# Kernel optimization log

Hardware: AMD Instinct MI355X
Metric: run time of the kernel (lower is better)

## Reference

```python
import jax, jax.numpy as jnp
import numpy as np

EPS = 1e-3  # tfa GroupNormalization default epsilon
H = 8       # num heads


def group_norm(x, gamma, beta):
    # x: [..., E]; per-sample group norm over each group of head_dim channels
    lead, E = x.shape[:-1], x.shape[-1]
    D = E // H
    xg = x.reshape(lead + (H, D))
    mu = xg.mean(-1, keepdims=True)
    var = xg.var(-1, keepdims=True)
    xg = (xg - mu) * jax.lax.rsqrt(var + EPS)
    xg = xg * gamma.reshape(H, D) + beta.reshape(H, D)
    return xg.reshape(lead + (E,))


def in_proj(x, W, b, gamma, beta):
    # Dense -> CELU(alpha=1) == ELU -> GroupNorm(groups=H)
    return group_norm(jax.nn.elu(x @ W + b), gamma, beta)


def setup_inputs() -> dict:
    B, M, E, MID = 16, 2048, 1024, 64
    D = E // H
    ks = jax.random.split(jax.random.key(0), 16)
    w = lambda k, shape: jax.random.normal(k, shape, jnp.float32) * 0.02
    inp = {
        "query": jax.random.normal(ks[0], (B, E), jnp.float32),
        "key": jax.random.normal(ks[1], (B * M, E), jnp.float32),
        "mask": jnp.ones((B, M), jnp.float32),
        "value1": jax.random.normal(ks[2], (B, E), jnp.float32),
        "value2": jax.random.normal(ks[3], (B * M, E), jnp.float32),
        # four in-projection layers: Dense(E,E) + GroupNorm gamma/beta
        "Wq": w(ks[4], (E, E)), "bq": jnp.zeros((E,), jnp.float32), "gq": jnp.ones((E,), jnp.float32), "Bq": jnp.zeros((E,), jnp.float32),
        "Wk": w(ks[5], (E, E)), "bk": jnp.zeros((E,), jnp.float32), "gk": jnp.ones((E,), jnp.float32), "Bk": jnp.zeros((E,), jnp.float32),
        "Wv1": w(ks[6], (E, E)), "bv1": jnp.zeros((E,), jnp.float32), "gv1": jnp.ones((E,), jnp.float32), "Bv1": jnp.zeros((E,), jnp.float32),
        "Wv2": w(ks[7], (E, E)), "bv2": jnp.zeros((E,), jnp.float32), "gv2": jnp.ones((E,), jnp.float32), "Bv2": jnp.zeros((E,), jnp.float32),
        # XLASCAtt: basic Dense(head_dim->64)+ReLU; last Dense(64->1); last2 Dense(64->head_dim)
        "Wb": w(ks[8], (D, MID)), "bb": jnp.zeros((MID,), jnp.float32),
        "Wl1": w(ks[9], (MID, 1)), "bl1": jnp.zeros((1,), jnp.float32),
        "Wl2": w(ks[10], (MID, D)), "bl2": jnp.zeros((D,), jnp.float32),
    }
    return inp


def reference(query, key, mask, value1, value2,
              Wq, bq, gq, Bq, Wk, bk, gk, Bk,
              Wv1, bv1, gv1, Bv1, Wv2, bv2, gv2, Bv2,
              Wb, bb, Wl1, bl1, Wl2, bl2):
    B, E = query.shape
    D = E // H
    # in-projections
    q = in_proj(query, Wq, bq, gq, Bq).reshape(B, H, D)            # [B,H,D]
    v1 = in_proj(value1, Wv1, bv1, gv1, Bv1).reshape(B, H, D)      # [B,H,D]
    k = in_proj(key, Wk, bk, gk, Bk).reshape(B, -1, H, D).transpose(0, 2, 1, 3)       # [B,H,M,D]
    v2 = in_proj(value2, Wv2, bv2, gv2, Bv2).reshape(B, -1, H, D).transpose(0, 2, 1, 3)  # [B,H,M,D]

    # low-rank bilinear attention map: elementwise q*k per head
    att_map = q[:, :, None, :] * k                                 # [B,H,M,D]
    basic = jax.nn.relu(att_map @ Wb + bb)                         # [B,H,M,MID]

    # masked mean-pool over memory positions
    m_ext = mask[:, None, :, None]                                 # [B,1,M,1]
    pool = (basic * m_ext).sum(-2) / m_ext.sum(-2)                 # [B,H,MID]

    # spatial attention (softmax over M) and channel gate (sigmoid)
    alpha_sp = (basic @ Wl1 + bl1)[..., 0]                         # [B,H,M]
    alpha_sp = jnp.where(mask[:, None, :] == 0, -1e9, alpha_sp)
    alpha_sp = jax.nn.softmax(alpha_sp, axis=-1)
    alpha_ch = jax.nn.sigmoid(pool @ Wl2 + bl2)                    # [B,H,D]

    v2_agg = jnp.einsum('bhm,bhmd->bhd', alpha_sp, v2)             # [B,H,D]
    attn = v1 * v2_agg * alpha_ch                                  # [B,H,D]
    return attn.reshape(B, H * D)
```

## Files before the change

### kernel.cpp

```cpp
#include <hip/hip_runtime.h>
#include <hip/hip_bf16.h>
#include <math.h>

typedef __attribute__((ext_vector_type(8))) short bf16x8;
typedef __attribute__((ext_vector_type(4))) float f32x4;
typedef __attribute__((ext_vector_type(8))) unsigned short u16x8;

typedef const float* fptr;
typedef const unsigned short* bfp;

__device__ inline float b2f(unsigned short u) {
    union { unsigned int i; float f; } v; v.i = ((unsigned int)u) << 16; return v.f;
}
__device__ inline unsigned short f2b(float x) {
    __hip_bfloat16 h = __float2bfloat16(x);
    return *(unsigned short*)&h;
}
__device__ inline float elu_f(float x) { return x > 0.f ? x : __expf(x) - 1.f; }

__device__ inline void load_lds16(const void* g, void* l) {
    __builtin_amdgcn_global_load_lds(
        (const __attribute__((address_space(1))) unsigned int*)g,
        (__attribute__((address_space(3))) unsigned int*)l, 16, 0, 0);
}

__global__ __launch_bounds__(256) void prep(
    fptr Wk, fptr Wv2, unsigned short* WtK, unsigned short* WtV2,
    fptr Wb, unsigned short* Wbt,
    fptr query, fptr Wq, fptr bq, fptr gq, fptr Bq,
    fptr value1, fptr Wv1, fptr bv1, fptr gv1, fptr Bv1,
    float* qws, float* v1ws)
{
    __shared__ __align__(16) char smem[16640];
    int blk = blockIdx.x, t = threadIdx.x;

    if (blk == 0) {
        unsigned short* tb = (unsigned short*)smem;
        for (int i = 0; i < 32; i++) {
            int idx = i * 256 + t;
            tb[(idx & 63) * 128 + (idx >> 6)] = f2b(Wb[idx]);
        }
        __syncthreads();
        for (int i = 0; i < 4; i++) {
            int o = (i * 256 + t) * 8;
            *(u16x8*)&Wbt[o] = *(const u16x8*)&tb[o];
        }
        return;
    }
    if (blk < 257) {
        float* xs = (float*)smem;
        float (*part)[128] = (float (*)[128])(smem + 4096);
        float (*r4)[2] = (float (*)[2])(smem + 4096 + 1024);
        int idx = blk - 1;
        int hgrp = idx & 7;
        int row  = (idx >> 3) & 15;
        int which = idx >> 7;
        fptr x  = which ? value1 : query;
        fptr W  = which ? Wv1 : Wq;
        fptr bi = which ? bv1 : bq;
        fptr g  = which ? gv1 : gq;
        fptr be = which ? Bv1 : Bq;
        float* outp = which ? v1ws : qws;
        int lane = t & 63, wv = t >> 6;
        for (int i = t; i < 1024; i += 256) xs[i] = x[row * 1024 + i];
        __syncthreads();
        int cl = t & 127, kh = t >> 7;
        int col = hgrp * 128 + cl;
        float acc = 0.f;
        const float* wp = W + (size_t)(kh * 512) * 1024 + col;
        for (int k = 0; k < 512; k++) acc += xs[kh * 512 + k] * wp[(size_t)k * 1024];
        part[kh][cl] = acc;
        __syncthreads();
        float e = 0.f;
        if (t < 128) e = elu_f(part[0][t] + part[1][t] + bi[col]);
        float s = e, ss = e * e;
        for (int m = 32; m > 0; m >>= 1) { s += __shfl_xor(s, m); ss += __shfl_xor(ss, m); }
        if (lane == 0) { r4[wv][0] = s; r4[wv][1] = ss; }
        __syncthreads();
        float S  = r4[0][0] + r4[1][0] + r4[2][0] + r4[3][0];
        float SS = r4[0][1] + r4[1][1] + r4[2][1] + r4[3][1];
        float mean = S * (1.f / 128.f);
        float var  = SS * (1.f / 128.f) - mean * mean;
        float inv  = rsqrtf(var + 1e-3f);
        if (t < 128) outp[row * 1024 + col] = (e - mean) * inv * g[col] + be[col];
        return;
    }
    {
        float (*tl)[65] = (float (*)[65])smem;
        int idx = blk - 257;
        fptr W = (idx >> 8) ? Wv2 : Wk;
        unsigned short* Wt = (idx >> 8) ? WtV2 : WtK;
        int k0 = ((idx >> 4) & 15) * 64, n0 = (idx & 15) * 64;
        #pragma unroll
        for (int i = 0; i < 16; i++) {
            int kl = i * 4 + (t >> 6), nl = t & 63;
            tl[kl][nl] = W[(size_t)(k0 + kl) * 1024 + n0 + nl];
        }
        __syncthreads();
        #pragma unroll
        for (int i = 0; i < 2; i++) {
            int nl = i * 32 + (t >> 3), kl8 = (t & 7) * 8;
            u16x8 o;
            #pragma unroll
            for (int e = 0; e < 8; e++) o[e] = f2b(tl[kl8 + e][nl]);
            *(u16x8*)&Wt[(size_t)(n0 + nl) * 1024 + k0 + kl8] = o;
        }
    }
}

__global__ __launch_bounds__(256, 4) void gemm_fused(
    fptr AKf, bfp WtK, fptr bkp, fptr gkp, fptr Bkp,
    fptr AVf, bfp WtV, fptr bvp, fptr gvp, fptr Bvp,
    bfp Wbt, const float* qws, fptr maskp, fptr bbp, fptr Wl1, fptr bl1,
    float* logits, float* poolpart, __hip_bfloat16* Z)
{
    __shared__ __align__(16) unsigned short pool[17408];
    unsigned short (*As)[128][32] = (unsigned short (*)[128][32])pool;
    unsigned short (*Bs)[128][32] = (unsigned short (*)[128][32])(pool + 8192);
    unsigned short (*Tt)[136]     = (unsigned short (*)[136])pool;
    __shared__ float sstat[128][2][2];
    __shared__ float masksh[128];
    __shared__ float poolred[4][64];

    int bid = blockIdx.x;
    int xcd = bid & 7;
    int seq = bid >> 3;
    int grp = seq >> 3;
    int h   = seq & 7;
    int which = grp >> 5;
    int rowtile = xcd * 32 + (grp & 31);

    int r0 = rowtile * 128;
    int n0 = h * 128;
    int b  = r0 >> 11;
    int mloc = r0 & 2047;
    int mt = rowtile & 15;
    int t = threadIdx.x, lane = t & 63, w = t >> 6;
    int c = lane & 15, q = lane >> 4;
    int rowbase = (w & 1) * 64, colbase = (w >> 1) * 64;

    fptr Af   = which ? AVf : AKf;
    bfp Wt    = which ? WtV : WtK;
    fptr bias = which ? bvp : bkp;
    fptr g    = which ? gvp : gkp;
    fptr be   = which ? Bvp : Bkp;

    if (which == 0 && t < 128) masksh[t] = maskp[r0 + t];

    f32x4 acc[4][4];
    const f32x4 fzero = {0.f, 0.f, 0.f, 0.f};
    #pragma unroll
    for (int i = 0; i < 4; i++)
        #pragma unroll
        for (int j = 0; j < 4; j++) acc[i][j] = fzero;

    int srow = lane >> 2;
    int sseg = (lane & 3) * 8;
    const float* agf = Af + (size_t)(r0 + w * 32 + srow) * 1024 + sseg;
    const unsigned short* bg = Wt + (size_t)(n0 + w * 32 + srow) * 1024 + sseg;

    for (int k0 = 0; k0 < 1024; k0 += 64) {
        load_lds16(bg + k0,                  &Bs[0][w * 32][0]);
        load_lds16(bg + k0 + 16 * 1024,      &Bs[0][w * 32 + 16][0]);
        load_lds16(bg + k0 + 32,             &Bs[1][w * 32][0]);
        load_lds16(bg + k0 + 32 + 16 * 1024, &Bs[1][w * 32 + 16][0]);
        #pragma unroll
        for (int ch = 0; ch < 4; ch++) {
            const float* src = agf + k0 + (ch & 1) * 16 * 1024 + (ch >> 1) * 32;
            float4 f0 = *(const float4*)src;
            float4 f1 = *(const float4*)(src + 4);
            u16x8 hv = { f2b(f0.x), f2b(f0.y), f2b(f0.z), f2b(f0.w),
                         f2b(f1.x), f2b(f1.y), f2b(f1.z), f2b(f1.w) };
            *(u16x8*)&As[ch >> 1][w * 32 + (ch & 1) * 16 + srow][sseg] = hv;
        }
        __syncthreads();
        #pragma unroll
        for (int p = 0; p < 2; p++) {
            bf16x8 af[4], bfv[4];
            #pragma unroll
            for (int i = 0; i < 4; i++) af[i]  = *(const bf16x8*)&As[p][rowbase + i * 16 + c][q * 8];
            #pragma unroll
            for (int j = 0; j < 4; j++) bfv[j] = *(const bf16x8*)&Bs[p][colbase + j * 16 + c][q * 8];
            #pragma unroll
            for (int i = 0; i < 4; i++)
                #pragma unroll
                for (int j = 0; j < 4; j++)
                    acc[i][j] = __builtin_amdgcn_mfma_f32_16x16x32_bf16(af[i], bfv[j], acc[i][j], 0, 0, 0);
        }
        __syncthreads();
    }

    float bcol[4], gcol[4], Bcol[4];
    #pragma unroll
    for (int j = 0; j < 4; j++) {
        int cg = n0 + colbase + j * 16 + c;
        bcol[j] = bias[cg]; gcol[j] = g[cg]; Bcol[j] = be[cg];
    }
    #pragma unroll
    for (int i = 0; i < 4; i++)
        #pragma unroll
        for (int j = 0; j < 4; j++)
            #pragma unroll
            for (int r = 0; r < 4; r++)
                acc[i][j][r] = elu_f(acc[i][j][r] + bcol[j]);
    #pragma unroll
    for (int i = 0; i < 4; i++) {
        #pragma unroll
        for (int r = 0; r < 4; r++) {
            float s  = acc[i][0][r] + acc[i][1][r] + acc[i][2][r] + acc[i][3][r];
            float ss = acc[i][0][r] * acc[i][0][r] + acc[i][1][r] * acc[i][1][r]
                     + acc[i][2][r] * acc[i][2][r] + acc[i][3][r] * acc[i][3][r];
            for (int m = 1; m < 16; m <<= 1) { s += __shfl_xor(s, m); ss += __shfl_xor(ss, m); }
            if (c == 0) {
                int rl = rowbase + i * 16 + q * 4 + r;
                sstat[rl][w >> 1][0] = s;
                sstat[rl][w >> 1][1] = ss;
            }
        }
    }
    __syncthreads();
    #pragma unroll
    for (int i = 0; i < 4; i++) {
        #pragma unroll
        for (int r = 0; r < 4; r++) {
            int rl = rowbase + i * 16 + q * 4 + r;
            float S  = sstat[rl][0][0] + sstat[rl][1][0];
            float SS = sstat[rl][0][1] + sstat[rl][1][1];
            float mean = S * (1.f / 128.f);
            float var  = SS * (1.f / 128.f) - mean * mean;
            float inv  = rsqrtf(var + 1e-3f);
            #pragma unroll
            for (int j = 0; j < 4; j++) {
                int cl = colbase + j * 16 + c;
                float v = (acc[i][j][r] - mean) * inv * gcol[j] + Bcol[j];
                Tt[rl][cl] = f2b(v);
            }
        }
    }
    __syncthreads();
    if (which != 0) {
        unsigned short* Zu = (unsigned short*)Z;
        #pragma unroll
        for (int i = 0; i < 8; i++) {
            int idx2 = i * 256 + t;
            int row = idx2 >> 4, ch = (idx2 & 15) * 8;
            *(u16x8*)&Zu[(size_t)(r0 + row) * 1024 + n0 + ch] = *(const u16x8*)&Tt[row][ch];
        }
        return;
    }

    const float* qrow = qws + b * 1024 + h * 128;
    f32x4 acc2[2][4];
    #pragma unroll
    for (int i = 0; i < 2; i++)
        #pragma unroll
        for (int j = 0; j < 4; j++) acc2[i][j] = fzero;
    #pragma unroll
    for (int s = 0; s < 4; s++) {
        bf16x8 af2[2], bfv[4];
        float qv[8];
        #pragma unroll
        for (int e = 0; e < 8; e++) qv[e] = qrow[s * 32 + q * 8 + e];
        #pragma unroll
        for (int i = 0; i < 2; i++)
            af2[i] = *(const bf16x8*)&Tt[w * 32 + i * 16 + c][s * 32 + q * 8];
        #pragma unroll
        for (int j = 0; j < 4; j++) {
            bf16x8 wv = *(const bf16x8*)&Wbt[(j * 16 + c) * 128 + s * 32 + q * 8];
            bf16x8 bv;
            #pragma unroll
            for (int e = 0; e < 8; e++)
                bv[e] = (short)f2b(b2f((unsigned short)wv[e]) * qv[e]);
            bfv[j] = bv;
        }
        #pragma unroll
        for (int i = 0; i < 2; i++)
            #pragma unroll
            for (int j = 0; j < 4; j++)
                acc2[i][j] = __builtin_amdgcn_mfma_f32_16x16x32_bf16(af2[i], bfv[j], acc2[i][j], 0, 0, 0);
    }

    float bbs[4], wl1s[4];
    #pragma unroll
    for (int j = 0; j < 4; j++) { bbs[j] = bbp[j * 16 + c]; wl1s[j] = Wl1[j * 16 + c]; }
    float bl1v = bl1[0];
    float pp[4] = {0.f, 0.f, 0.f, 0.f};
    #pragma unroll
    for (int i = 0; i < 2; i++) {
        #pragma unroll
        for (int r = 0; r < 4; r++) {
            int ml = w * 32 + i * 16 + q * 4 + r;
            float mv = masksh[ml];
            float lg = 0.f;
            #pragma unroll
            for (int j = 0; j < 4; j++) {
                float basic = fmaxf(acc2[i][j][r] + bbs[j], 0.f);
                lg += basic * wl1s[j];
                pp[j] += basic * mv;
            }
            lg += __shfl_xor(lg, 1); lg += __shfl_xor(lg, 2);
            lg += __shfl_xor(lg, 4); lg += __shfl_xor(lg, 8);
            if (c == 0)
                logits[((size_t)(b * 8 + h)) * 2048 + mloc + ml] = lg + bl1v;
        }
    }
    #pragma unroll
    for (int j = 0; j < 4; j++) {
        pp[j] += __shfl_xor(pp[j], 16);
        pp[j] += __shfl_xor(pp[j], 32);
    }
    if (lane < 16) {
        #pragma unroll
        for (int j = 0; j < 4; j++) poolred[w][j * 16 + c] = pp[j];
    }
    __syncthreads();
    if (t < 64) {
        float p = poolred[0][t] + poolred[1][t] + poolred[2][t] + poolred[3][t];
        poolpart[((size_t)((b * 8 + h) * 16 + mt)) * 64 + t] = p;
    }
}

__global__ __launch_bounds__(512) void finalize_fused(
    const float* logits, const float* poolpart, fptr maskp,
    const __hip_bfloat16* v2buf, const float* v1ws,
    fptr Wl2, fptr bl2, float* out)
{
    __shared__ float alph[2048];
    __shared__ float red[8];
    __shared__ float redm[8];
    __shared__ float pools[64];
    __shared__ float ach[128];
    __shared__ float redl[8][128];
    int h = blockIdx.x, b = blockIdx.y;
    int t = threadIdx.x, lane = t & 63, wv = t >> 6;

    const float* lg = logits + (size_t)(b * 8 + h) * 2048;
    float msum_l = 0.f, mx_l = -1e30f;
    for (int i = t; i < 2048; i += 512) {
        float mv = maskp[b * 2048 + i];
        msum_l += mv;
        float v = (mv == 0.f) ? -1e9f : lg[i];
        alph[i] = v;
        mx_l = fmaxf(mx_l, v);
    }
    for (int mm = 32; mm > 0; mm >>= 1) {
        msum_l += __shfl_xor(msum_l, mm);
        mx_l = fmaxf(mx_l, __shfl_xor(mx_l, mm));
    }
    if (lane == 0) { red[wv] = msum_l; redm[wv] = mx_l; }
    __syncthreads();
    float msum = 0.f, mx = -1e30f;
    #pragma unroll
    for (int i = 0; i < 8; i++) { msum += red[i]; mx = fmaxf(mx, redm[i]); }

    float se = 0.f;
    for (int i = t; i < 2048; i += 512) {
        float e = __expf(alph[i] - mx);
        alph[i] = e;
        se += e;
    }
    for (int mm = 32; mm > 0; mm >>= 1) se += __shfl_xor(se, mm);
    __syncthreads();
    if (lane == 0) red[wv] = se;
    __syncthreads();
    float S = 0.f;
    #pragma unroll
    for (int i = 0; i < 8; i++) S += red[i];
    float invS = 1.f / S;
    for (int i = t; i < 2048; i += 512) alph[i] *= invS;

    if (t < 64) {
        const float* pq = poolpart + ((size_t)(b * 8 + h) * 16) * 64 + t;
        float p = 0.f;
        for (int pt = 0; pt < 16; pt++) p += pq[pt * 64];
        pools[t] = p / msum;
    }
    __syncthreads();
    if (t < 128) {
        float s2 = bl2[t];
        for (int mid = 0; mid < 64; mid++) s2 += pools[mid] * Wl2[mid * 128 + t];
        ach[t] = 1.f / (1.f + __expf(-s2));
    }
    __syncthreads();

    int mo = lane >> 4, d8 = (lane & 15) * 8;
    float acc[8] = {};
    for (int it = 0; it < 64; it++) {
        int m = it * 32 + wv * 4 + mo;
        bf16x8 v8 = *(const bf16x8*)&v2buf[((size_t)(b * 2048 + m)) * 1024 + h * 128 + d8];
        float a = alph[m];
        #pragma unroll
        for (int j = 0; j < 8; j++)
            acc[j] += a * b2f(((unsigned short*)&v8)[j]);
    }
    #pragma unroll
    for (int j = 0; j < 8; j++) {
        acc[j] += __shfl_xor(acc[j], 16);
        acc[j] += __shfl_xor(acc[j], 32);
    }
    if (lane < 16) {
        #pragma unroll
        for (int j = 0; j < 8; j++) redl[wv][d8 + j] = acc[j];
    }
    __syncthreads();
    if (t < 128) {
        float s = 0.f;
        #pragma unroll
        for (int i = 0; i < 8; i++) s += redl[i][t];
        out[b * 1024 + h * 128 + t] = v1ws[b * 1024 + h * 128 + t] * s * ach[t];
    }
}

extern "C" void kernel_launch(void* const* d_in, const int* in_sizes, int n_in,
                              void* d_out, int out_size, void* d_ws, size_t ws_size,
                              hipStream_t stream) {
    fptr query  = (fptr)d_in[0];
    fptr key    = (fptr)d_in[1];
    fptr maskp  = (fptr)d_in[2];
    fptr value1 = (fptr)d_in[3];
    fptr value2 = (fptr)d_in[4];
    fptr Wq = (fptr)d_in[5],  bq = (fptr)d_in[6],  gq = (fptr)d_in[7],  Bq = (fptr)d_in[8];
    fptr Wk = (fptr)d_in[9],  bk = (fptr)d_in[10], gk = (fptr)d_in[11], Bk = (fptr)d_in[12];
    fptr Wv1 = (fptr)d_in[13], bv1 = (fptr)d_in[14], gv1 = (fptr)d_in[15], Bv1 = (fptr)d_in[16];
    fptr Wv2 = (fptr)d_in[17], bv2 = (fptr)d_in[18], gv2 = (fptr)d_in[19], Bv2 = (fptr)d_in[20];
    fptr Wb = (fptr)d_in[21], bb = (fptr)d_in[22];
    fptr Wl1 = (fptr)d_in[23], bl1 = (fptr)d_in[24];
    fptr Wl2 = (fptr)d_in[25], bl2 = (fptr)d_in[26];

    const size_t MB = 1024 * 1024;
    char* w = (char*)d_ws;
    __hip_bfloat16* zV2   = (__hip_bfloat16*)w;
    unsigned short* WtK   = (unsigned short*)(w + 64 * MB);
    unsigned short* WtV2  = (unsigned short*)(w + 66 * MB);
    unsigned short* Wbt   = (unsigned short*)(w + 68 * MB);
    float* qws      = (float*)(w + 68 * MB + 65536);
    float* v1ws     = qws + 16 * 1024;
    float* logits   = v1ws + 16 * 1024;
    float* poolpart = logits + 16 * 8 * 2048;
    float* out = (float*)d_out;

    hipLaunchKernelGGL(prep, dim3(769), dim3(256), 0, stream,
                       Wk, Wv2, WtK, WtV2, Wb, Wbt,
                       query, Wq, bq, gq, Bq, value1, Wv1, bv1, gv1, Bv1,
                       qws, v1ws);
    hipLaunchKernelGGL(gemm_fused, dim3(4096), dim3(256), 0, stream,
                       key, (bfp)WtK, bk, gk, Bk,
                       value2, (bfp)WtV2, bv2, gv2, Bv2,
                       (bfp)Wbt, qws, maskp, bb, Wl1, bl1, logits, poolpart, zV2);
    hipLaunchKernelGGL(finalize_fused, dim3(8, 16), dim3(512), 0, stream,
                       logits, poolpart, maskp, zV2, v1ws, Wl2, bl2, out);
}
```

Before: 529.9 us.

## Register-prefetch double-buffered GEMM main loop with XOR-swizzled LDS layout

Restructures the K/V2 projection GEMM main loop from 64-wide steps with direct global-to-LDS loads into 32-wide steps. Each step prefetches the next tile into registers and writes it into the alternate LDS buffer while MFMAs run on the current one, leaving a single barrier per iteration. The LDS columns are XOR-swizzled on write and read to reduce bank conflicts. The small query/value1 projection loop also gets an unroll pragma. This hides global load latency but raises register pressure, and the smaller K step doubles the number of barriers.

Result: no change. 540.0 us (+1.9%).

```diff
diff --git a/kernel.cpp b/kernel.cpp
--- a/kernel.cpp
+++ b/kernel.cpp
@@ -17,12 +17,6 @@
     return *(unsigned short*)&h;
 }
 __device__ inline float elu_f(float x) { return x > 0.f ? x : __expf(x) - 1.f; }
-
-__device__ inline void load_lds16(const void* g, void* l) {
-    __builtin_amdgcn_global_load_lds(
-        (const __attribute__((address_space(1))) unsigned int*)g,
-        (__attribute__((address_space(3))) unsigned int*)l, 16, 0, 0);
-}
 
 __global__ __launch_bounds__(256) void prep(
     fptr Wk, fptr Wv2, unsigned short* WtK, unsigned short* WtV2,
@@ -68,6 +62,7 @@
         int col = hgrp * 128 + cl;
         float acc = 0.f;
         const float* wp = W + (size_t)(kh * 512) * 1024 + col;
+        #pragma unroll 8
         for (int k = 0; k < 512; k++) acc += xs[kh * 512 + k] * wp[(size_t)k * 1024];
         part[kh][cl] = acc;
         __syncthreads();
@@ -156,39 +151,62 @@
 
     int srow = lane >> 2;
     int sseg = (lane & 3) * 8;
+    int swcol = ((lane & 3) ^ ((lane >> 3) & 3)) * 8;
+    int sq8 = (q ^ ((c >> 1) & 3)) * 8;
+
     const float* agf = Af + (size_t)(r0 + w * 32 + srow) * 1024 + sseg;
     const unsigned short* bg = Wt + (size_t)(n0 + w * 32 + srow) * 1024 + sseg;
 
-    for (int k0 = 0; k0 < 1024; k0 += 64) {
-        load_lds16(bg + k0,                  &Bs[0][w * 32][0]);
-        load_lds16(bg + k0 + 16 * 1024,      &Bs[0][w * 32 + 16][0]);
-        load_lds16(bg + k0 + 32,             &Bs[1][w * 32][0]);
-        load_lds16(bg + k0 + 32 + 16 * 1024, &Bs[1][w * 32 + 16][0]);
-        #pragma unroll
-        for (int ch = 0; ch < 4; ch++) {
-            const float* src = agf + k0 + (ch & 1) * 16 * 1024 + (ch >> 1) * 32;
-            float4 f0 = *(const float4*)src;
-            float4 f1 = *(const float4*)(src + 4);
-            u16x8 hv = { f2b(f0.x), f2b(f0.y), f2b(f0.z), f2b(f0.w),
-                         f2b(f1.x), f2b(f1.y), f2b(f1.z), f2b(f1.w) };
-            *(u16x8*)&As[ch >> 1][w * 32 + (ch & 1) * 16 + srow][sseg] = hv;
-        }
-        __syncthreads();
-        #pragma unroll
-        for (int p = 0; p < 2; p++) {
-            bf16x8 af[4], bfv[4];
-            #pragma unroll
-            for (int i = 0; i < 4; i++) af[i]  = *(const bf16x8*)&As[p][rowbase + i * 16 + c][q * 8];
-            #pragma unroll
-            for (int j = 0; j < 4; j++) bfv[j] = *(const bf16x8*)&Bs[p][colbase + j * 16 + c][q * 8];
-            #pragma unroll
-            for (int i = 0; i < 4; i++)
-                #pragma unroll
-                for (int j = 0; j < 4; j++)
-                    acc[i][j] = __builtin_amdgcn_mfma_f32_16x16x32_bf16(af[i], bfv[j], acc[i][j], 0, 0, 0);
-        }
-        __syncthreads();
-    }
+    float4 ra0, ra1, ra2, ra3;
+    u16x8 rb0, rb1;
+
+#define LOAD_TILE(K0) do { \
+        ra0 = *(const float4*)(agf + (K0)); \
+        ra1 = *(const float4*)(agf + (K0) + 4); \
+        ra2 = *(const float4*)(agf + (K0) + 16 * 1024); \
+        ra3 = *(const float4*)(agf + (K0) + 16 * 1024 + 4); \
+        rb0 = *(const u16x8*)(bg + (K0)); \
+        rb1 = *(const u16x8*)(bg + (K0) + 16 * 1024); \
+    } while (0)
+
+#define WRITE_TILE(BUF) do { \
+        u16x8 h0 = { f2b(ra0.x), f2b(ra0.y), f2b(ra0.z), f2b(ra0.w), \
+                     f2b(ra1.x), f2b(ra1.y), f2b(ra1.z), f2b(ra1.w) }; \
+        u16x8 h1 = { f2b(ra2.x), f2b(ra2.y), f2b(ra2.z), f2b(ra2.w), \
+                     f2b(ra3.x), f2b(ra3.y), f2b(ra3.z), f2b(ra3.w) }; \
+        *(u16x8*)&As[BUF][w * 32 + srow][swcol] = h0; \
+        *(u16x8*)&As[BUF][w * 32 + 16 + srow][swcol] = h1; \
+        *(u16x8*)&Bs[BUF][w * 32 + srow][swcol] = rb0; \
+        *(u16x8*)&Bs[BUF][w * 32 + 16 + srow][swcol] = rb1; \
+    } while (0)
+
+    LOAD_TILE(0);
+    WRITE_TILE(0);
+    LOAD_TILE(32);
+    __syncthreads();
+
+    #pragma unroll 2
+    for (int k = 0; k < 32; k++) {
+        int cur = k & 1;
+        if (k < 31) {
+            WRITE_TILE(cur ^ 1);
+            if (k < 30) LOAD_TILE((k + 2) * 32);
+        }
+        bf16x8 af[4], bfv[4];
+        #pragma unroll
+        for (int i = 0; i < 4; i++) af[i]  = *(const bf16x8*)&As[cur][rowbase + i * 16 + c][sq8];
+        #pragma unroll
+        for (int j = 0; j < 4; j++) bfv[j] = *(const bf16x8*)&Bs[cur][colbase + j * 16 + c][sq8];
+        #pragma unroll
+        for (int i = 0; i < 4; i++)
+            #pragma unroll
+            for (int j = 0; j < 4; j++)
+                acc[i][j] = __builtin_amdgcn_mfma_f32_16x16x32_bf16(af[i], bfv[j], acc[i][j], 0, 0, 0);
+        __syncthreads();
+    }
+
+#undef LOAD_TILE
+#undef WRITE_TILE
 
     float bcol[4], gcol[4], Bcol[4];
     #pragma unroll
```
